# Kernel tuning notes

Hardware: AMD Instinct MI355X
Metric: run time of the kernel (lower is better)

Reference implementation:

```python
import jax, jax.numpy as jnp
import numpy as np

EPS = 1e-5

def conv1d(x, w, b, pad):
    # x: (B,Cin,T), w: (Cout,Cin,K)
    y = jax.lax.conv_general_dilated(x, w, (1,), [(pad, pad)],
                                     dimension_numbers=('NCW', 'OIW', 'NCW'))
    return y + b[None, :, None]

def group_norm(x, scale, bias, groups):
    B, C, T = x.shape
    xg = x.reshape(B, groups, C // groups, T)
    mu = xg.mean(axis=(2, 3), keepdims=True)
    var = xg.var(axis=(2, 3), keepdims=True)
    xn = ((xg - mu) * jax.lax.rsqrt(var + EPS)).reshape(B, C, T)
    return xn * scale[None, :, None] + bias[None, :, None]

def setup_inputs() -> dict:
    key = jax.random.key(0)
    ks = jax.random.split(key, 16)
    T, B = 1024, 128
    class_size, style_size, char_style_size = 80, 256, 64
    hidden, n_out = 128, 1
    cin = class_size + style_size + char_style_size  # 400
    def w(k, shape, fan_in):
        return jax.random.normal(k, shape, jnp.float32) * (1.0 / np.sqrt(fan_in))
    inp = {
        'input': jax.random.normal(ks[0], (T, B, class_size), jnp.float32),
        'g_style': jax.random.normal(ks[1], (B, style_size), jnp.float32),
        'spacing_style': jax.random.normal(ks[2], (B, 8), jnp.float32),
        'char_style': jax.random.normal(ks[3], (B, class_size, char_style_size), jnp.float32),
        'conv1_w': w(ks[4], (hidden, cin, 3), cin * 3),
        'conv1_b': jnp.zeros((hidden,), jnp.float32),
        'gn1_s': jnp.ones((hidden,), jnp.float32),
        'gn1_b': jnp.zeros((hidden,), jnp.float32),
        'conv2_w': w(ks[5], (hidden // 2, hidden, 3), hidden * 3),
        'conv2_b': jnp.zeros((hidden // 2,), jnp.float32),
        'gn2_s': jnp.ones((hidden // 2,), jnp.float32),
        'gn2_b': jnp.zeros((hidden // 2,), jnp.float32),
        'conv3_w': w(ks[6], (hidden // 4, hidden // 2, 3), (hidden // 2) * 3),
        'conv3_b': jnp.zeros((hidden // 4,), jnp.float32),
        'gn3_s': jnp.ones((hidden // 4,), jnp.float32),
        'gn3_b': jnp.zeros((hidden // 4,), jnp.float32),
        'conv4_w': w(ks[7], (n_out, hidden // 4, 1), hidden // 4),
        'conv4_b': jnp.zeros((n_out,), jnp.float32),
        'mean': jnp.full((1, n_out), 2.0, jnp.float32),
        'std': jnp.full((1, n_out), 1.0, jnp.float32),
    }
    return inp

def reference(input, g_style, spacing_style, char_style,
              conv1_w, conv1_b, gn1_s, gn1_b,
              conv2_w, conv2_b, gn2_s, gn2_b,
              conv3_w, conv3_b, gn3_s, gn3_b,
              conv4_w, conv4_b, mean, std):
    T, B, _ = input.shape
    # vectorized char-style gather (replaces the python double loop)
    text_chars = jnp.argmax(input, axis=2)                      # (T,B)
    input_style = char_style[jnp.arange(B)[None, :], text_chars]  # (T,B,Dc)
    gs = jnp.broadcast_to(g_style[None], (T,) + g_style.shape)    # (T,B,Ds)
    x = jnp.concatenate([input, gs, input_style], axis=2)         # (T,B,Cin)
    x = x.transpose(1, 2, 0)                                      # (B,Cin,T)
    x = jax.nn.relu(group_norm(conv1d(x, conv1_w, conv1_b, 1), gn1_s, gn1_b, 32))
    x = jax.nn.relu(group_norm(conv1d(x, conv2_w, conv2_b, 1), gn2_s, gn2_b, 32))
    x = jax.nn.relu(group_norm(conv1d(x, conv3_w, conv3_b, 1), gn3_s, gn3_b, 32))
    x = conv1d(x, conv4_w, conv4_b, 0)                            # (B,n_out,T)
    out = x.transpose(2, 0, 1)                                    # (T,B,n_out)
    return out * std + mean
```

## Files before the change

### kernel.cpp

```cpp
#include <hip/hip_runtime.h>
#include <hip/hip_bf16.h>

#define T_LEN 1024
#define BATCH 128
#define NM 131072

typedef __attribute__((ext_vector_type(8))) short short8;
typedef __attribute__((ext_vector_type(4))) float f32x4;

__device__ __forceinline__ float b2f(ushort u) {
  union { uint i; float f; } c; c.i = ((uint)u) << 16; return c.f;
}
__device__ __forceinline__ ushort f2b(float f) {
  __hip_bfloat16 h = __float2bfloat16(f);
  return *reinterpret_cast<ushort*>(&h);
}
__device__ __forceinline__ uint pack2(float a, float b) {
  return (uint)f2b(a) | ((uint)f2b(b) << 16);
}

__global__ __launch_bounds__(256) void k_prep(const float* __restrict__ inp, const float* __restrict__ cs,
    const float* __restrict__ gsty,
    const float* __restrict__ w1, const float* __restrict__ b1,
    const float* __restrict__ w2, const float* __restrict__ w3,
    ushort* __restrict__ X1c, float* __restrict__ Gfull, float* __restrict__ Gk0, float* __restrict__ Gk2,
    ushort* __restrict__ Wp1, ushort* __restrict__ Wp2, ushort* __restrict__ Wp3) {
  int bid = blockIdx.x, tid = threadIdx.x;
  if (bid < 1024) {
    __shared__ __align__(16) ushort Lc[4][32][64];
    int b0 = (bid >> 5) * 4;
    int t0 = (bid & 31) * 32;
    int q = tid & 3;
    int u = tid >> 2;
    int bp = u & 3;
    int tpA = u >> 2, tpB = tpA + 16;
    int mA = (t0 + tpA)*128 + b0 + bp;
    int mB = (t0 + tpB)*128 + b0 + bp;
    const float* rpA = inp + (size_t)mA*80 + q*20;
    const float* rpB = inp + (size_t)mB*80 + q*20;
    float va[20], vb[20];
    #pragma unroll
    for (int i = 0; i < 5; ++i) {
      float4 ua = *(const float4*)(rpA + i*4);
      va[i*4+0]=ua.x; va[i*4+1]=ua.y; va[i*4+2]=ua.z; va[i*4+3]=ua.w;
    }
    #pragma unroll
    for (int i = 0; i < 5; ++i) {
      float4 ub = *(const float4*)(rpB + i*4);
      vb[i*4+0]=ub.x; vb[i*4+1]=ub.y; vb[i*4+2]=ub.z; vb[i*4+3]=ub.w;
    }
    {
      float best = va[0]; int bi = q*20;
      #pragma unroll
      for (int i = 1; i < 20; ++i) if (va[i] > best) { best = va[i]; bi = q*20 + i; }
      #pragma unroll
      for (int d = 1; d <= 2; d <<= 1) {
        float ob = __shfl_xor(best, d);
        int   oi = __shfl_xor(bi, d);
        if (ob > best || (ob == best && oi < bi)) { best = ob; bi = oi; }
      }
      ushort* lr = &Lc[bp][tpA][0];
      const float* crow = cs + ((size_t)(b0+bp)*80 + bi)*64 + q*16;
      #pragma unroll
      for (int i = 0; i < 4; ++i) {
        float4 uu = *(const float4*)(crow + i*4);
        uint2 pk; pk.x = pack2(uu.x, uu.y); pk.y = pack2(uu.z, uu.w);
        *(uint2*)(lr + q*16 + i*4) = pk;
      }
    }
    {
      float best = vb[0]; int bi = q*20;
      #pragma unroll
      for (int i = 1; i < 20; ++i) if (vb[i] > best) { best = vb[i]; bi = q*20 + i; }
      #pragma unroll
      for (int d = 1; d <= 2; d <<= 1) {
        float ob = __shfl_xor(best, d);
        int   oi = __shfl_xor(bi, d);
        if (ob > best || (ob == best && oi < bi)) { best = ob; bi = oi; }
      }
      ushort* lr = &Lc[bp][tpB][0];
      const float* crow = cs + ((size_t)(b0+bp)*80 + bi)*64 + q*16;
      #pragma unroll
      for (int i = 0; i < 4; ++i) {
        float4 uu = *(const float4*)(crow + i*4);
        uint2 pk; pk.x = pack2(uu.x, uu.y); pk.y = pack2(uu.z, uu.w);
        *(uint2*)(lr + q*16 + i*4) = pk;
      }
    }
    __syncthreads();
    int wave = tid >> 6, lane = tid & 63;
    ushort* dst = X1c + ((size_t)(b0 + wave)*1024 + t0)*64;
    const ushort* src = &Lc[wave][0][0];
    #pragma unroll
    for (int it = 0; it < 4; ++it) {
      int r = it*64 + lane;
      *(uint4*)(dst + r*8) = *(const uint4*)(src + r*8);
    }
  } else if (bid < 1152) {
    int b = bid - 1024;
    __shared__ float gl[256];
    gl[tid] = gsty[b*256 + tid];
    __syncthreads();
    if (tid < 128) {
      int o = tid;
      const float* wr = w1 + (size_t)o*1200 + 240;
      float s0 = 0.f, s1 = 0.f, s2 = 0.f;
      for (int c = 0; c < 256; ++c) {
        float g = gl[c];
        s0 += wr[c*3+0]*g; s1 += wr[c*3+1]*g; s2 += wr[c*3+2]*g;
      }
      Gk0[b*128+o] = s0;
      Gk2[b*128+o] = s2;
      Gfull[b*128+o] = s0 + s1 + s2 + b1[o];
    }
  } else {
    int e = (bid - 1152)*256 + tid;
    if (e < 61440) {
      int o = e / 480, r = e % 480, k = r / 160, c = r % 160;
      float v = 0.f;
      if (c < 80)       v = w1[(size_t)o*1200 + c*3 + k];
      else if (c >= 96) v = w1[(size_t)o*1200 + (336 + (c-96))*3 + k];
      Wp1[e] = f2b(v);
    } else if (e < 61440 + 24576) {
      int e2 = e - 61440;
      int o = e2/384, r = e2%384, k = r/128, c = r%128;
      Wp2[e2] = f2b(w2[(size_t)o*384 + c*3 + k]);
    } else if (e < 61440 + 24576 + 6144) {
      int e3 = e - 61440 - 24576;
      int o = e3/192, r = e3%192, k = r/64, c = r%64;
      Wp3[e3] = f2b(w3[(size_t)o*192 + c*3 + k]);
    }
  }
}

__device__ __forceinline__ void c1_ldf(const float* __restrict__ inp, int b, int cc, int t0, int task,
                                       float4& fa, float4& fb) {
  int r = task >> 2, q = task & 3;
  int t = t0 - 1 + r;
  int c8 = cc*32 + q*8;
  fa = make_float4(0.f,0.f,0.f,0.f); fb = fa;
  if (t >= 0 && t < T_LEN && c8 < 80) {
    const float* src = inp + ((size_t)t*BATCH + b)*80 + c8;
    fa = *(const float4*)src;
    fb = *(const float4*)(src + 4);
  }
}
__device__ __forceinline__ uint4 c1_ldc(const ushort* X1cb, int cc, int t0, int task) {
  int r = task >> 2, q = task & 3;
  int t = t0 - 1 + r;
  if (t >= 0 && t < T_LEN) return *(const uint4*)(X1cb + (size_t)t*64 + (cc-3)*32 + q*8);
  return make_uint4(0u,0u,0u,0u);
}
__device__ __forceinline__ uint4 packf(float4 a, float4 b) {
  uint4 p;
  p.x = pack2(a.x, a.y); p.y = pack2(a.z, a.w);
  p.z = pack2(b.x, b.y); p.w = pack2(b.z, b.w);
  return p;
}
__device__ __forceinline__ short8 c1_ldw(const ushort* Wp1, int cc, int task) {
  int o = task / 12, seg = task % 12;
  int k = seg >> 2, oct = seg & 3;
  return *(const short8*)(Wp1 + (size_t)o*480 + k*160 + cc*32 + oct*8);
}
__device__ __forceinline__ void c1_wrx(ushort (*Xsb)[40], int task, uint4 v) {
  int r = task >> 2, q = task & 3;
  *(uint4*)&Xsb[r][q*8] = v;
}
__device__ __forceinline__ void c1_wrw(ushort (*Wsb)[104], int task, short8 v) {
  int o = task / 12, seg = task % 12;
  *(short8*)&Wsb[o][seg*8] = v;
}

__global__ __launch_bounds__(256) void k_conv1(const float* __restrict__ inp, const ushort* __restrict__ X1c,
    const ushort* __restrict__ Wp1,
    const float* __restrict__ Gfull, const float* __restrict__ Gk0, const float* __restrict__ Gk2,
    ushort* __restrict__ y1, float2* __restrict__ part1) {
  __shared__ __align__(16) ushort Xs[2][130][40];
  __shared__ __align__(16) ushort Ws[2][128][104];
  __shared__ float gf[128], g0v[128], g2v[128];
  __shared__ float ps[4][128], pq[4][128];
  int b = blockIdx.x, tt = blockIdx.y;
  int t0 = tt * 128;
  int tid = threadIdx.x, lane = tid & 63, wave = tid >> 6;
  int ln = lane & 15, lq = lane >> 4, wt = wave * 32;
  const ushort* X1cb = X1c + (size_t)b * 65536;

  if (tid < 128) {
    gf[tid]  = Gfull[b*128 + tid];
    g0v[tid] = Gk0[b*128 + tid];
    g2v[tid] = Gk2[b*128 + tid];
  }
  f32x4 acc[2][8];
  #pragma unroll
  for (int m = 0; m < 2; ++m)
    #pragma unroll
    for (int n = 0; n < 8; ++n) { f32x4 z = {0.f,0.f,0.f,0.f}; acc[m][n] = z; }

  float4 fa0, fb0, fa1, fb1, fa2, fb2;
  uint4 rx0, rx1, rx2;
  short8 rw[6];

  c1_ldf(inp, b, 0, t0, tid, fa0, fb0);
  c1_ldf(inp, b, 0, t0, tid + 256, fa1, fb1);
  if (tid < 8) c1_ldf(inp, b, 0, t0, tid + 512, fa2, fb2);
  #pragma unroll
  for (int i = 0; i < 6; ++i) rw[i] = c1_ldw(Wp1, 0, tid + i*256);
  c1_wrx(Xs[0], tid, packf(fa0, fb0));
  c1_wrx(Xs[0], tid + 256, packf(fa1, fb1));
  if (tid < 8) c1_wrx(Xs[0], tid + 512, packf(fa2, fb2));
  #pragma unroll
  for (int i = 0; i < 6; ++i) c1_wrw(Ws[0], tid + i*256, rw[i]);
  __syncthreads();

  for (int cc = 0; cc < 5; ++cc) {
    bool more = (cc < 4);
    bool nf = (cc + 1 < 3);
    if (more) {
      if (nf) {
        c1_ldf(inp, b, cc+1, t0, tid, fa0, fb0);
        c1_ldf(inp, b, cc+1, t0, tid + 256, fa1, fb1);
        if (tid < 8) c1_ldf(inp, b, cc+1, t0, tid + 512, fa2, fb2);
      } else {
        rx0 = c1_ldc(X1cb, cc+1, t0, tid);
        rx1 = c1_ldc(X1cb, cc+1, t0, tid + 256);
        if (tid < 8) rx2 = c1_ldc(X1cb, cc+1, t0, tid + 512);
      }
      #pragma unroll
      for (int i = 0; i < 6; ++i) rw[i] = c1_ldw(Wp1, cc+1, tid + i*256);
    }
    int cur = cc & 1;
    #pragma unroll
    for (int k = 0; k < 3; ++k) {
      short8 a0 = *(const short8*)&Xs[cur][wt + ln + k][lq*8];
      short8 a1 = *(const short8*)&Xs[cur][wt + 16 + ln + k][lq*8];
      #pragma unroll
      for (int nt = 0; nt < 8; ++nt) {
        short8 bb = *(const short8*)&Ws[cur][nt*16 + ln][k*32 + lq*8];
        acc[0][nt] = __builtin_amdgcn_mfma_f32_16x16x32_bf16(a0, bb, acc[0][nt], 0, 0, 0);
        acc[1][nt] = __builtin_amdgcn_mfma_f32_16x16x32_bf16(a1, bb, acc[1][nt], 0, 0, 0);
      }
    }
    if (more) {
      int nxt = cur ^ 1;
      if (nf) {
        c1_wrx(Xs[nxt], tid, packf(fa0, fb0));
        c1_wrx(Xs[nxt], tid + 256, packf(fa1, fb1));
        if (tid < 8) c1_wrx(Xs[nxt], tid + 512, packf(fa2, fb2));
      } else {
        c1_wrx(Xs[nxt], tid, rx0);
        c1_wrx(Xs[nxt], tid + 256, rx1);
        if (tid < 8) c1_wrx(Xs[nxt], tid + 512, rx2);
      }
      #pragma unroll
      for (int i = 0; i < 6; ++i) c1_wrw(Ws[nxt], tid + i*256, rw[i]);
    }
    __syncthreads();
  }

  #pragma unroll
  for (int nt = 0; nt < 8; ++nt) {
    int o = nt*16 + ln;
    float add = gf[o];
    float s = 0.f, sq = 0.f;
    #pragma unroll
    for (int mt = 0; mt < 2; ++mt) {
      int tb = t0 + wt + mt*16 + lq*4;
      float vv[4];
      #pragma unroll
      for (int r = 0; r < 4; ++r) {
        float v = acc[mt][nt][r] + add;
        int t = tb + r;
        if (t == 0) v -= g0v[o];
        if (t == T_LEN-1) v -= g2v[o];
        vv[r] = v; s += v; sq += v*v;
      }
      uint2 pk;
      pk.x = pack2(vv[0], vv[1]);
      pk.y = pack2(vv[2], vv[3]);
      *(uint2*)(y1 + ((size_t)b*128 + o)*T_LEN + tb) = pk;
    }
    s  += __shfl_xor(s, 16);  s  += __shfl_xor(s, 32);
    sq += __shfl_xor(sq, 16); sq += __shfl_xor(sq, 32);
    if (lane < 16) { ps[wave][o] = s; pq[wave][o] = sq; }
  }
  __syncthreads();
  if (tid < 128) {
    float S = ps[0][tid]+ps[1][tid]+ps[2][tid]+ps[3][tid];
    float Q = pq[0][tid]+pq[1][tid]+pq[2][tid]+pq[3][tid];
    part1[((size_t)b*128 + tid)*8 + tt] = make_float2(S, Q);
  }
}

__device__ __forceinline__ short8 mid_ldw(const ushort* Wp, int cin, int cc, int task) {
  int o = task / 12, seg = task % 12;
  int k = seg >> 2, oct = seg & 3;
  return *(const short8*)(Wp + ((size_t)o*3 + k)*cin + cc*32 + oct*8);
}
__device__ __forceinline__ void mid_wrw(ushort (*Wsb)[104], int task, short8 v) {
  int o = task / 12, seg = task % 12;
  *(short8*)&Wsb[o][seg*8] = v;
}

template<int NC, int CO, int NT, int CPG>
__global__ __launch_bounds__(256) void k_convmid(const ushort* __restrict__ xin,
    const ushort* __restrict__ Wp, const float* __restrict__ bias,
    const float2* __restrict__ partin, const float* __restrict__ gs, const float* __restrict__ gb,
    ushort* __restrict__ yout, float2* __restrict__ part) {
  constexpr int CIN = NC*32;
  constexpr int NG = CIN/CPG;
  __shared__ __align__(16) ushort Xs[2][130][40];
  __shared__ __align__(16) ushort Ws[2][CO][104];
  __shared__ float2 affl[CIN];
  __shared__ float ssb[CIN], qqb[CIN];
  __shared__ float2 gmr[NG];
  __shared__ float bl[CO];
  __shared__ float ps[4][CO], pq[4][CO];
  int b = blockIdx.x, tt = blockIdx.y, t0 = tt*128;
  int tid = threadIdx.x, lane = tid & 63, wave = tid >> 6;
  int ln = lane & 15, lq = lane >> 4, wt = wave*32;
  int cp = (tid & 15)*2, j = tid >> 4;
  int er = (tid < 32) ? 0 : 129, eci = tid & 31;
  const ushort* xb = xin + (size_t)b * CIN * T_LEN;

  if (tid < CIN) {
    const float2* p = partin + (size_t)(b*CIN + tid)*8;
    float S = 0.f, Q = 0.f;
    #pragma unroll
    for (int j2 = 0; j2 < 8; ++j2) { float2 v = p[j2]; S += v.x; Q += v.y; }
    ssb[tid] = S; qqb[tid] = Q;
  }
  if (tid < CO)  bl[tid]  = bias[tid];

  f32x4 acc[2][NT];
  #pragma unroll
  for (int m = 0; m < 2; ++m)
    #pragma unroll
    for (int n = 0; n < NT; ++n) { f32x4 z = {0.f,0.f,0.f,0.f}; acc[m][n] = z; }

  short8 v0, v1;
  ushort ev = 0;
  short8 rw0, rw1, rw2;
  int te = t0 - 1 + er;

  {
    const ushort* s0 = xb + (size_t)cp * T_LEN + t0 + j*8;
    v0 = *(const short8*)s0;
    v1 = *(const short8*)(s0 + T_LEN);
    ev = 0;
    if (tid < 64 && te >= 0 && te < T_LEN) ev = xb[(size_t)eci * T_LEN + te];
    rw0 = mid_ldw(Wp, CIN, 0, tid);
    if constexpr (CO == 64) {
      rw1 = mid_ldw(Wp, CIN, 0, tid + 256);
      rw2 = mid_ldw(Wp, CIN, 0, tid + 512);
    } else {
      if (tid < 128) rw1 = mid_ldw(Wp, CIN, 0, tid + 256);
    }
  }
  __syncthreads();
  if (tid < NG) {
    float S = 0.f, Q = 0.f;
    #pragma unroll
    for (int ci = 0; ci < CPG; ++ci) { S += ssb[tid*CPG+ci]; Q += qqb[tid*CPG+ci]; }
    float invn = 1.f / (float)(CPG * T_LEN);
    float m = S * invn;
    float var = Q * invn - m*m;
    gmr[tid] = make_float2(m, rsqrtf(var + 1e-5f));
  }
  __syncthreads();
  if (tid < CIN) {
    float2 mr = gmr[tid / CPG];
    float a = mr.y * gs[tid];
    affl[tid] = make_float2(a, gb[tid] - mr.x * a);
  }
  __syncthreads();
  {
    float2 A0 = affl[cp], A1 = affl[cp+1];
    #pragma unroll
    for (int e = 0; e < 8; ++e) {
      float f0 = fmaxf(0.f, b2f((ushort)v0[e])*A0.x + A0.y);
      float f1 = fmaxf(0.f, b2f((ushort)v1[e])*A1.x + A1.y);
      *(uint*)&Xs[0][1 + j*8 + e][cp] = pack2(f0, f1);
    }
    if (tid < 64) {
      ushort val = 0;
      if (te >= 0 && te < T_LEN) { float2 A = affl[eci]; val = f2b(fmaxf(0.f, b2f(ev)*A.x + A.y)); }
      Xs[0][er][eci] = val;
    }
    mid_wrw(Ws[0], tid, rw0);
    if constexpr (CO == 64) {
      mid_wrw(Ws[0], tid + 256, rw1);
      mid_wrw(Ws[0], tid + 512, rw2);
    } else {
      if (tid < 128) mid_wrw(Ws[0], tid + 256, rw1);
    }
  }
  __syncthreads();

  for (int cc = 0; cc < NC; ++cc) {
    bool more = (cc + 1 < NC);
    if (more) {
      const ushort* s0 = xb + (size_t)((cc+1)*32 + cp) * T_LEN + t0 + j*8;
      v0 = *(const short8*)s0;
      v1 = *(const short8*)(s0 + T_LEN);
      ev = 0;
      if (tid < 64 && te >= 0 && te < T_LEN) ev = xb[(size_t)((cc+1)*32 + eci) * T_LEN + te];
      rw0 = mid_ldw(Wp, CIN, cc+1, tid);
      if constexpr (CO == 64) {
        rw1 = mid_ldw(Wp, CIN, cc+1, tid + 256);
        rw2 = mid_ldw(Wp, CIN, cc+1, tid + 512);
      } else {
        if (tid < 128) rw1 = mid_ldw(Wp, CIN, cc+1, tid + 256);
      }
    }
    int cur = cc & 1;
    #pragma unroll
    for (int k = 0; k < 3; ++k) {
      short8 a0 = *(const short8*)&Xs[cur][wt + ln + k][lq*8];
      short8 a1 = *(const short8*)&Xs[cur][wt + 16 + ln + k][lq*8];
      #pragma unroll
      for (int nt = 0; nt < NT; ++nt) {
        short8 bb = *(const short8*)&Ws[cur][nt*16 + ln][k*32 + lq*8];
        acc[0][nt] = __builtin_amdgcn_mfma_f32_16x16x32_bf16(a0, bb, acc[0][nt], 0, 0, 0);
        acc[1][nt] = __builtin_amdgcn_mfma_f32_16x16x32_bf16(a1, bb, acc[1][nt], 0, 0, 0);
      }
    }
    if (more) {
      int nxt = cur ^ 1;
      float2 A0 = affl[(cc+1)*32 + cp], A1 = affl[(cc+1)*32 + cp + 1];
      #pragma unroll
      for (int e = 0; e < 8; ++e) {
        float f0 = fmaxf(0.f, b2f((ushort)v0[e])*A0.x + A0.y);
        float f1 = fmaxf(0.f, b2f((ushort)v1[e])*A1.x + A1.y);
        *(uint*)&Xs[nxt][1 + j*8 + e][cp] = pack2(f0, f1);
      }
      if (tid < 64) {
        ushort val = 0;
        if (te >= 0 && te < T_LEN) { float2 A = affl[(cc+1)*32 + eci]; val = f2b(fmaxf(0.f, b2f(ev)*A.x + A.y)); }
        Xs[nxt][er][eci] = val;
      }
      mid_wrw(Ws[nxt], tid, rw0);
      if constexpr (CO == 64) {
        mid_wrw(Ws[nxt], tid + 256, rw1);
        mid_wrw(Ws[nxt], tid + 512, rw2);
      } else {
        if (tid < 128) mid_wrw(Ws[nxt], tid + 256, rw1);
      }
    }
    __syncthreads();
  }

  #pragma unroll
  for (int nt = 0; nt < NT; ++nt) {
    int o = nt*16 + ln;
    float add = bl[o];
    float s = 0.f, sq = 0.f;
    #pragma unroll
    for (int mt = 0; mt < 2; ++mt) {
      int tb = t0 + wt + mt*16 + lq*4;
      float vv[4];
      #pragma unroll
      for (int r = 0; r < 4; ++r) {
        float v = acc[mt][nt][r] + add;
        vv[r] = v; s += v; sq += v*v;
      }
      uint2 pk;
      pk.x = pack2(vv[0], vv[1]);
      pk.y = pack2(vv[2], vv[3]);
      *(uint2*)(yout + ((size_t)b*CO + o)*T_LEN + tb) = pk;
    }
    s  += __shfl_xor(s, 16);  s  += __shfl_xor(s, 32);
    sq += __shfl_xor(sq, 16); sq += __shfl_xor(sq, 32);
    if (lane < 16) { ps[wave][o] = s; pq[wave][o] = sq; }
  }
  __syncthreads();
  if (tid < CO) {
    float S = ps[0][tid]+ps[1][tid]+ps[2][tid]+ps[3][tid];
    float Q = pq[0][tid]+pq[1][tid]+pq[2][tid]+pq[3][tid];
    part[((size_t)b*CO + tid)*8 + tt] = make_float2(S, Q);
  }
}

__global__ __launch_bounds__(256) void k_final(const ushort* __restrict__ y3, const float2* __restrict__ part3,
    const float* __restrict__ s3, const float* __restrict__ b3,
    const float* __restrict__ w4, const float* __restrict__ b4,
    const float* __restrict__ mn, const float* __restrict__ sd, float* __restrict__ out) {
  int b = blockIdx.x;
  int t = blockIdx.y * 256 + threadIdx.x;
  __shared__ float wl[32];
  __shared__ float2 al[32];
  if (threadIdx.x < 32) {
    int c = threadIdx.x;
    const float2* p = part3 + (size_t)(b*32 + c)*8;
    float S = 0.f, Q = 0.f;
    #pragma unroll
    for (int j = 0; j < 8; ++j) { float2 v = p[j]; S += v.x; Q += v.y; }
    float invn = 1.f / (float)T_LEN;
    float m = S * invn;
    float var = Q * invn - m*m;
    float rs = rsqrtf(var + 1e-5f);
    float a = rs * s3[c];
    al[c] = make_float2(a, b3[c] - m*a);
    wl[c] = w4[c];
  }
  __syncthreads();
  float s = b4[0];
  #pragma unroll 8
  for (int c = 0; c < 32; ++c) {
    float v = b2f(y3[((size_t)b*32 + c)*T_LEN + t]);
    float2 A = al[c];
    s += wl[c] * fmaxf(0.f, v*A.x + A.y);
  }
  out[(size_t)t*BATCH + b] = s*sd[0] + mn[0];
}

extern "C" void kernel_launch(void* const* d_in, const int* in_sizes, int n_in,
                              void* d_out, int out_size, void* d_ws, size_t ws_size,
                              hipStream_t stream) {
  const float* inp  = (const float*)d_in[0];
  const float* gsty = (const float*)d_in[1];
  const float* cs   = (const float*)d_in[3];
  const float* w1   = (const float*)d_in[4];
  const float* b1   = (const float*)d_in[5];
  const float* gn1s = (const float*)d_in[6];
  const float* gn1b = (const float*)d_in[7];
  const float* w2   = (const float*)d_in[8];
  const float* b2   = (const float*)d_in[9];
  const float* gn2s = (const float*)d_in[10];
  const float* gn2b = (const float*)d_in[11];
  const float* w3   = (const float*)d_in[12];
  const float* b3   = (const float*)d_in[13];
  const float* gn3s = (const float*)d_in[14];
  const float* gn3b = (const float*)d_in[15];
  const float* w4   = (const float*)d_in[16];
  const float* b4   = (const float*)d_in[17];
  const float* mn   = (const float*)d_in[18];
  const float* sd   = (const float*)d_in[19];
  float* out = (float*)d_out;
  ushort* wsu = (ushort*)d_ws;

  ushort* X1c = wsu;
  ushort* Wp1 = X1c + (size_t)8388608;
  ushort* Wp2 = Wp1 + 61440;
  ushort* Wp3 = Wp2 + 24576;
  float* Gfull = (float*)(Wp3 + 6144);
  float* Gk0   = Gfull + 16384;
  float* Gk2   = Gk0 + 16384;
  ushort* y1 = (ushort*)(Gk2 + 16384);
  ushort* y2 = y1 + (size_t)NM*128;
  ushort* y3 = y2 + (size_t)NM*64;
  float2* part1 = (float2*)(y3 + (size_t)NM*32);
  float2* part2 = part1 + 131072;
  float2* part3 = part2 + 65536;

  k_prep<<<1512, 256, 0, stream>>>(inp, cs, gsty, w1, b1, w2, w3,
                                   X1c, Gfull, Gk0, Gk2, Wp1, Wp2, Wp3);
  k_conv1<<<dim3(128,8), 256, 0, stream>>>(inp, X1c, Wp1, Gfull, Gk0, Gk2, y1, part1);
  k_convmid<4,64,4,4><<<dim3(128,8), 256, 0, stream>>>(y1, Wp2, b2, part1, gn1s, gn1b, y2, part2);
  k_convmid<2,32,2,2><<<dim3(128,8), 256, 0, stream>>>(y2, Wp3, b3, part2, gn2s, gn2b, y3, part3);
  k_final<<<dim3(128,4), 256, 0, stream>>>(y3, part3, gn3s, gn3b, w4, b4, mn, sd, out);
}
```

Baseline: 95.56 us.

## Gather char-style rows inside conv1 using argmax indices instead of materializing X1c

The prep kernel now writes only the per-(t,b) argmax index instead of building a bf16 char-style activation tensor in workspace. conv1 loads the indices into shared memory and gathers the fp32 char_style rows directly while staging its input tiles, converting them to bf16 on the fly. This removes the write and re-read of a 16 MB intermediate. In exchange, conv1 performs indirect gathers from a small char_style table, which is likely cache-resident, and an extra shared-memory index load.

```diff
diff --git a/kernel.cpp b/kernel.cpp
--- a/kernel.cpp
+++ b/kernel.cpp
@@ -19,15 +19,14 @@
   return (uint)f2b(a) | ((uint)f2b(b) << 16);
 }
 
-__global__ __launch_bounds__(256) void k_prep(const float* __restrict__ inp, const float* __restrict__ cs,
+__global__ __launch_bounds__(256) void k_prep(const float* __restrict__ inp,
     const float* __restrict__ gsty,
     const float* __restrict__ w1, const float* __restrict__ b1,
     const float* __restrict__ w2, const float* __restrict__ w3,
-    ushort* __restrict__ X1c, float* __restrict__ Gfull, float* __restrict__ Gk0, float* __restrict__ Gk2,
+    int* __restrict__ idx, float* __restrict__ Gfull, float* __restrict__ Gk0, float* __restrict__ Gk2,
     ushort* __restrict__ Wp1, ushort* __restrict__ Wp2, ushort* __restrict__ Wp3) {
   int bid = blockIdx.x, tid = threadIdx.x;
   if (bid < 1024) {
-    __shared__ __align__(16) ushort Lc[4][32][64];
     int b0 = (bid >> 5) * 4;
     int t0 = (bid & 31) * 32;
     int q = tid & 3;
@@ -59,14 +58,7 @@
         int   oi = __shfl_xor(bi, d);
         if (ob > best || (ob == best && oi < bi)) { best = ob; bi = oi; }
       }
-      ushort* lr = &Lc[bp][tpA][0];
-      const float* crow = cs + ((size_t)(b0+bp)*80 + bi)*64 + q*16;
-      #pragma unroll
-      for (int i = 0; i < 4; ++i) {
-        float4 uu = *(const float4*)(crow + i*4);
-        uint2 pk; pk.x = pack2(uu.x, uu.y); pk.y = pack2(uu.z, uu.w);
-        *(uint2*)(lr + q*16 + i*4) = pk;
-      }
+      if (q == 0) idx[mA] = bi;
     }
     {
       float best = vb[0]; int bi = q*20;
@@ -78,23 +70,7 @@
         int   oi = __shfl_xor(bi, d);
         if (ob > best || (ob == best && oi < bi)) { best = ob; bi = oi; }
       }
-      ushort* lr = &Lc[bp][tpB][0];
-      const float* crow = cs + ((size_t)(b0+bp)*80 + bi)*64 + q*16;
-      #pragma unroll
-      for (int i = 0; i < 4; ++i) {
-        float4 uu = *(const float4*)(crow + i*4);
-        uint2 pk; pk.x = pack2(uu.x, uu.y); pk.y = pack2(uu.z, uu.w);
-        *(uint2*)(lr + q*16 + i*4) = pk;
-      }
-    }
-    __syncthreads();
-    int wave = tid >> 6, lane = tid & 63;
-    ushort* dst = X1c + ((size_t)(b0 + wave)*1024 + t0)*64;
-    const ushort* src = &Lc[wave][0][0];
-    #pragma unroll
-    for (int it = 0; it < 4; ++it) {
-      int r = it*64 + lane;
-      *(uint4*)(dst + r*8) = *(const uint4*)(src + r*8);
+      if (q == 0) idx[mB] = bi;
     }
   } else if (bid < 1152) {
     int b = bid - 1024;
@@ -133,23 +109,25 @@
   }
 }
 
-__device__ __forceinline__ void c1_ldf(const float* __restrict__ inp, int b, int cc, int t0, int task,
+__device__ __forceinline__ void c1_ldg(const float* __restrict__ inp, const float* __restrict__ cs,
+                                       const int* idxs, int b, int cc, int t0, int task,
                                        float4& fa, float4& fb) {
   int r = task >> 2, q = task & 3;
   int t = t0 - 1 + r;
-  int c8 = cc*32 + q*8;
   fa = make_float4(0.f,0.f,0.f,0.f); fb = fa;
-  if (t >= 0 && t < T_LEN && c8 < 80) {
-    const float* src = inp + ((size_t)t*BATCH + b)*80 + c8;
+  if (t >= 0 && t < T_LEN) {
+    const float* src;
+    if (cc < 3) {
+      int c8 = cc*32 + q*8;
+      if (c8 >= 80) return;
+      src = inp + ((size_t)t*BATCH + b)*80 + c8;
+    } else {
+      int jc = idxs[r];
+      src = cs + ((size_t)b*80 + jc)*64 + (cc-3)*32 + q*8;
+    }
     fa = *(const float4*)src;
     fb = *(const float4*)(src + 4);
   }
-}
-__device__ __forceinline__ uint4 c1_ldc(const ushort* X1cb, int cc, int t0, int task) {
-  int r = task >> 2, q = task & 3;
-  int t = t0 - 1 + r;
-  if (t >= 0 && t < T_LEN) return *(const uint4*)(X1cb + (size_t)t*64 + (cc-3)*32 + q*8);
-  return make_uint4(0u,0u,0u,0u);
 }
 __device__ __forceinline__ uint4 packf(float4 a, float4 b) {
   uint4 p;
@@ -171,20 +149,24 @@
   *(short8*)&Wsb[o][seg*8] = v;
 }
 
-__global__ __launch_bounds__(256) void k_conv1(const float* __restrict__ inp, const ushort* __restrict__ X1c,
-    const ushort* __restrict__ Wp1,
+__global__ __launch_bounds__(256) void k_conv1(const float* __restrict__ inp, const float* __restrict__ cs,
+    const int* __restrict__ idx, const ushort* __restrict__ Wp1,
     const float* __restrict__ Gfull, const float* __restrict__ Gk0, const float* __restrict__ Gk2,
     ushort* __restrict__ y1, float2* __restrict__ part1) {
   __shared__ __align__(16) ushort Xs[2][130][40];
   __shared__ __align__(16) ushort Ws[2][128][104];
   __shared__ float gf[128], g0v[128], g2v[128];
   __shared__ float ps[4][128], pq[4][128];
+  __shared__ int idxs[130];
   int b = blockIdx.x, tt = blockIdx.y;
   int t0 = tt * 128;
   int tid = threadIdx.x, lane = tid & 63, wave = tid >> 6;
   int ln = lane & 15, lq = lane >> 4, wt = wave * 32;
-  const ushort* X1cb = X1c + (size_t)b * 65536;
-
+
+  if (tid < 130) {
+    int t = t0 - 1 + tid;
+    idxs[tid] = (t >= 0 && t < T_LEN) ? idx[t*BATCH + b] : 0;
+  }
   if (tid < 128) {
     gf[tid]  = Gfull[b*128 + tid];
     g0v[tid] = Gk0[b*128 + tid];
@@ -197,12 +179,11 @@
     for (int n = 0; n < 8; ++n) { f32x4 z = {0.f,0.f,0.f,0.f}; acc[m][n] = z; }
 
   float4 fa0, fb0, fa1, fb1, fa2, fb2;
-  uint4 rx0, rx1, rx2;
   short8 rw[6];
 
-  c1_ldf(inp, b, 0, t0, tid, fa0, fb0);
-  c1_ldf(inp, b, 0, t0, tid + 256, fa1, fb1);
-  if (tid < 8) c1_ldf(inp, b, 0, t0, tid + 512, fa2, fb2);
+  c1_ldg(inp, cs, idxs, b, 0, t0, tid, fa0, fb0);
+  c1_ldg(inp, cs, idxs, b, 0, t0, tid + 256, fa1, fb1);
+  if (tid < 8) c1_ldg(inp, cs, idxs, b, 0, t0, tid + 512, fa2, fb2);
   #pragma unroll
   for (int i = 0; i < 6; ++i) rw[i] = c1_ldw(Wp1, 0, tid + i*256);
   c1_wrx(Xs[0], tid, packf(fa0, fb0));
@@ -214,17 +195,10 @@
 
   for (int cc = 0; cc < 5; ++cc) {
     bool more = (cc < 4);
-    bool nf = (cc + 1 < 3);
     if (more) {
-      if (nf) {
-        c1_ldf(inp, b, cc+1, t0, tid, fa0, fb0);
-        c1_ldf(inp, b, cc+1, t0, tid + 256, fa1, fb1);
-        if (tid < 8) c1_ldf(inp, b, cc+1, t0, tid + 512, fa2, fb2);
-      } else {
-        rx0 = c1_ldc(X1cb, cc+1, t0, tid);
-        rx1 = c1_ldc(X1cb, cc+1, t0, tid + 256);
-        if (tid < 8) rx2 = c1_ldc(X1cb, cc+1, t0, tid + 512);
-      }
+      c1_ldg(inp, cs, idxs, b, cc+1, t0, tid, fa0, fb0);
+      c1_ldg(inp, cs, idxs, b, cc+1, t0, tid + 256, fa1, fb1);
+      if (tid < 8) c1_ldg(inp, cs, idxs, b, cc+1, t0, tid + 512, fa2, fb2);
       #pragma unroll
       for (int i = 0; i < 6; ++i) rw[i] = c1_ldw(Wp1, cc+1, tid + i*256);
     }
@@ -242,15 +216,9 @@
     }
     if (more) {
       int nxt = cur ^ 1;
-      if (nf) {
-        c1_wrx(Xs[nxt], tid, packf(fa0, fb0));
-        c1_wrx(Xs[nxt], tid + 256, packf(fa1, fb1));
-        if (tid < 8) c1_wrx(Xs[nxt], tid + 512, packf(fa2, fb2));
-      } else {
-        c1_wrx(Xs[nxt], tid, rx0);
-        c1_wrx(Xs[nxt], tid + 256, rx1);
-        if (tid < 8) c1_wrx(Xs[nxt], tid + 512, rx2);
-      }
+      c1_wrx(Xs[nxt], tid, packf(fa0, fb0));
+      c1_wrx(Xs[nxt], tid + 256, packf(fa1, fb1));
+      if (tid < 8) c1_wrx(Xs[nxt], tid + 512, packf(fa2, fb2));
       #pragma unroll
       for (int i = 0; i < 6; ++i) c1_wrw(Ws[nxt], tid + i*256, rw[i]);
     }
@@ -538,8 +506,8 @@
   float* out = (float*)d_out;
   ushort* wsu = (ushort*)d_ws;
 
-  ushort* X1c = wsu;
-  ushort* Wp1 = X1c + (size_t)8388608;
+  int*    idx = (int*)wsu;
+  ushort* Wp1 = wsu + (size_t)262144;
   ushort* Wp2 = Wp1 + 61440;
   ushort* Wp3 = Wp2 + 24576;
   float* Gfull = (float*)(Wp3 + 6144);
@@ -552,9 +520,9 @@
   float2* part2 = part1 + 131072;
   float2* part3 = part2 + 65536;
 
-  k_prep<<<1512, 256, 0, stream>>>(inp, cs, gsty, w1, b1, w2, w3,
-                                   X1c, Gfull, Gk0, Gk2, Wp1, Wp2, Wp3);
-  k_conv1<<<dim3(128,8), 256, 0, stream>>>(inp, X1c, Wp1, Gfull, Gk0, Gk2, y1, part1);
+  k_prep<<<1512, 256, 0, stream>>>(inp, gsty, w1, b1, w2, w3,
+                                   idx, Gfull, Gk0, Gk2, Wp1, Wp2, Wp3);
+  k_conv1<<<dim3(128,8), 256, 0, stream>>>(inp, cs, idx, Wp1, Gfull, Gk0, Gk2, y1, part1);
   k_convmid<4,64,4,4><<<dim3(128,8), 256, 0, stream>>>(y1, Wp2, b2, part1, gn1s, gn1b, y2, part2);
   k_convmid<2,32,2,2><<<dim3(128,8), 256, 0, stream>>>(y2, Wp3, b3, part2, gn2s, gn2b, y3, part3);
   k_final<<<dim3(128,4), 256, 0, stream>>>(y3, part3, gn3s, gn3b, w4, b4, mn, sd, out);
```

New measurement: 94.81 us. Within noise of the previous version (-0.8%).
